# Performance work log

Measured on AMD Instinct MI355X. Metric: run time of the kernel, lower is better.

## Reference

```python
import jax, jax.numpy as jnp
import numpy as np

EPS = 1e-05

def setup_inputs() -> dict:
    key = jax.random.key(0)
    k1, = jax.random.split(key, 1)
    x = jax.random.normal(k1, (4, 4096, 2048), dtype=jnp.float32)
    g = jnp.ones((2048,), dtype=jnp.float32)
    return {"x": x, "g": g}

def reference(x, g):
    # RMSNorm: x / sqrt(mean(x^2, axis=-1) + eps) * g, computed in fp32
    dtype = x.dtype
    xf = x.astype(jnp.float32)
    ms = jnp.mean(xf * xf, axis=-1, keepdims=True)  # [B,S,1]
    out = xf * jax.lax.rsqrt(ms + EPS) * g
    return out.astype(dtype)
```

## Files before the change

### kernel.cpp

```cpp
#include <hip/hip_runtime.h>

#define ROW_LEN 2048
#define BLOCK   256
#define EPS     1e-5f

__global__ __launch_bounds__(BLOCK) void RMSNorm_56607668961691_kernel(
    const float* __restrict__ x,
    const float* __restrict__ g,
    float* __restrict__ out)
{
    const int wave = threadIdx.x >> 6;
    const int lane = threadIdx.x & 63;
    const size_t row = (size_t)blockIdx.x * (BLOCK / 64) + wave;

    const float4* __restrict__ xr   = reinterpret_cast<const float4*>(x + row * ROW_LEN) + lane;
    float4* __restrict__       outr = reinterpret_cast<float4*>(out + row * ROW_LEN) + lane;
    const float4* __restrict__ gv   = reinterpret_cast<const float4*>(g) + lane;

    float4 v[8];
    float4 gr[8];
    #pragma unroll
    for (int j = 0; j < 8; ++j) v[j]  = xr[j * 64];
    #pragma unroll
    for (int j = 0; j < 8; ++j) gr[j] = gv[j * 64];

    __builtin_amdgcn_sched_barrier(0);

    float s0 = 0.f, s1 = 0.f, s2 = 0.f, s3 = 0.f;
    #pragma unroll
    for (int j = 0; j < 8; ++j) {
        s0 += v[j].x * v[j].x;
        s1 += v[j].y * v[j].y;
        s2 += v[j].z * v[j].z;
        s3 += v[j].w * v[j].w;
    }
    float ss = (s0 + s1) + (s2 + s3);

    #pragma unroll
    for (int off = 32; off > 0; off >>= 1)
        ss += __shfl_xor(ss, off, 64);

    const float scale = rsqrtf(ss * (1.0f / (float)ROW_LEN) + EPS);

    #pragma unroll
    for (int j = 0; j < 8; ++j) {
        float4 o;
        o.x = v[j].x * scale * gr[j].x;
        o.y = v[j].y * scale * gr[j].y;
        o.z = v[j].z * scale * gr[j].z;
        o.w = v[j].w * scale * gr[j].w;
        outr[j * 64] = o;
    }
}

extern "C" void kernel_launch(void* const* d_in, const int* in_sizes, int n_in,
                              void* d_out, int out_size, void* d_ws, size_t ws_size,
                              hipStream_t stream) {
    const float* x = (const float*)d_in[0];
    const float* g = (const float*)d_in[1];
    float* out = (float*)d_out;

    const int rows = in_sizes[0] / ROW_LEN;
    const int grid = rows / (BLOCK / 64);
    RMSNorm_56607668961691_kernel<<<grid, BLOCK, 0, stream>>>(x, g, out);
}
```

Before: 230.7 us.

## Double-buffer rows through LDS with async global_load_lds, eight rows per wave

Each wave now processes eight consecutive rows instead of one. The next row is prefetched into a second LDS buffer with global_load_lds while the current row is reduced and written out, and an explicit vmcnt wait gates each buffer. The aim is to overlap load latency with compute and stores, and to load the gamma vector once per eight rows instead of once per row. In exchange the grid shrinks eightfold and each block uses 64 KB of LDS, which limits resident waves per CU. Correctness relies on the hand-counted vmcnt values, which also count the outstanding stores.

```diff
diff --git a/kernel.cpp b/kernel.cpp
--- a/kernel.cpp
+++ b/kernel.cpp
@@ -1,55 +1,89 @@
 #include <hip/hip_runtime.h>
+#include <stdint.h>
 
 #define ROW_LEN 2048
+#define R4      512
 #define BLOCK   256
+#define NR      8
 #define EPS     1e-5f
+
+typedef __attribute__((address_space(1))) unsigned int u32_g;
+typedef __attribute__((address_space(3))) unsigned int u32_l;
+
+__device__ __forceinline__ void gload_lds16(const float4* src, float4* lds_dst) {
+    __builtin_amdgcn_global_load_lds((const u32_g*)(const void*)src,
+                                     (u32_l*)(void*)lds_dst, 16, 0, 0);
+}
 
 __global__ __launch_bounds__(BLOCK) void RMSNorm_56607668961691_kernel(
     const float* __restrict__ x,
     const float* __restrict__ g,
     float* __restrict__ out)
 {
+    __shared__ float4 lds[2][BLOCK / 64][R4];
+
     const int wave = threadIdx.x >> 6;
     const int lane = threadIdx.x & 63;
-    const size_t row = (size_t)blockIdx.x * (BLOCK / 64) + wave;
+    const size_t wid  = (size_t)blockIdx.x * (BLOCK / 64) + wave;
+    const size_t row0 = wid * NR;
 
-    const float4* __restrict__ xr   = reinterpret_cast<const float4*>(x + row * ROW_LEN) + lane;
-    float4* __restrict__       outr = reinterpret_cast<float4*>(out + row * ROW_LEN) + lane;
+    const float4* __restrict__ xr   = reinterpret_cast<const float4*>(x) + row0 * R4 + lane;
+    float4* __restrict__       outr = reinterpret_cast<float4*>(out)     + row0 * R4 + lane;
     const float4* __restrict__ gv   = reinterpret_cast<const float4*>(g) + lane;
 
-    float4 v[8];
+    #pragma unroll
+    for (int j = 0; j < 8; ++j)
+        gload_lds16(xr + j * 64, &lds[0][wave][j * 64]);
+
     float4 gr[8];
-    #pragma unroll
-    for (int j = 0; j < 8; ++j) v[j]  = xr[j * 64];
     #pragma unroll
     for (int j = 0; j < 8; ++j) gr[j] = gv[j * 64];
 
-    __builtin_amdgcn_sched_barrier(0);
+    #pragma unroll 1
+    for (int r = 0; r < NR; ++r) {
+        const int cur = r & 1;
 
-    float s0 = 0.f, s1 = 0.f, s2 = 0.f, s3 = 0.f;
-    #pragma unroll
-    for (int j = 0; j < 8; ++j) {
-        s0 += v[j].x * v[j].x;
-        s1 += v[j].y * v[j].y;
-        s2 += v[j].z * v[j].z;
-        s3 += v[j].w * v[j].w;
-    }
-    float ss = (s0 + s1) + (s2 + s3);
+        asm volatile("s_waitcnt vmcnt(8)" ::: "memory");
 
-    #pragma unroll
-    for (int off = 32; off > 0; off >>= 1)
-        ss += __shfl_xor(ss, off, 64);
+        float4 v[8];
+        #pragma unroll
+        for (int j = 0; j < 8; ++j) v[j] = lds[cur][wave][j * 64 + lane];
 
-    const float scale = rsqrtf(ss * (1.0f / (float)ROW_LEN) + EPS);
+        __builtin_amdgcn_sched_barrier(0);
 
-    #pragma unroll
-    for (int j = 0; j < 8; ++j) {
-        float4 o;
-        o.x = v[j].x * scale * gr[j].x;
-        o.y = v[j].y * scale * gr[j].y;
-        o.z = v[j].z * scale * gr[j].z;
-        o.w = v[j].w * scale * gr[j].w;
-        outr[j * 64] = o;
+        if (r + 1 < NR) {
+            const float4* xn = xr + (size_t)(r + 1) * R4;
+            #pragma unroll
+            for (int j = 0; j < 8; ++j)
+                gload_lds16(xn + j * 64, &lds[cur ^ 1][wave][j * 64]);
+        }
+
+        float s0 = 0.f, s1 = 0.f, s2 = 0.f, s3 = 0.f;
+        #pragma unroll
+        for (int j = 0; j < 8; ++j) {
+            s0 += v[j].x * v[j].x;
+            s1 += v[j].y * v[j].y;
+            s2 += v[j].z * v[j].z;
+            s3 += v[j].w * v[j].w;
+        }
+        float ss = (s0 + s1) + (s2 + s3);
+
+        #pragma unroll
+        for (int off = 32; off > 0; off >>= 1)
+            ss += __shfl_xor(ss, off, 64);
+
+        const float scale = rsqrtf(ss * (1.0f / (float)ROW_LEN) + EPS);
+
+        float4* o = outr + (size_t)r * R4;
+        #pragma unroll
+        for (int j = 0; j < 8; ++j) {
+            float4 ov;
+            ov.x = v[j].x * scale * gr[j].x;
+            ov.y = v[j].y * scale * gr[j].y;
+            ov.z = v[j].z * scale * gr[j].z;
+            ov.w = v[j].w * scale * gr[j].w;
+            o[j * 64] = ov;
+        }
     }
 }
 
@@ -61,6 +95,6 @@
     float* out = (float*)d_out;
 
     const int rows = in_sizes[0] / ROW_LEN;
-    const int grid = rows / (BLOCK / 64);
+    const int grid = rows / ((BLOCK / 64) * NR);
     RMSNorm_56607668961691_kernel<<<grid, BLOCK, 0, stream>>>(x, g, out);
 }
```

Measured after the change: 238.9 us. 3.6% more time.
